# Performance work log

Hardware: AMD Instinct MI355X
Metric: run time of the kernel (lower is better)

## Reference

```python
import jax, jax.numpy as jnp
import numpy as np
from jax import lax

E = 4; D_MODEL = 128; D_FF = 128; DT_RANK = 32; D_STATE = 16
L = 12; PAD = 12  # padding_factor=1.0 -> pad L extra zeros
K_TOP = 6; U = 1e-6; EPS = 1e-5
BATCH = 8; NODES = 307; BN = BATCH * NODES
FREQ_IN = (L + PAD) // 2 + 1 + K_TOP  # 19
FREQ_OUT = L // 2 + 1                 # 7


def setup_inputs() -> dict:
    key = jax.random.key(0)
    ks = jax.random.split(key, 14)
    x = jax.random.normal(ks[0], (BN, L, D_MODEL), jnp.float32)
    graph = jax.random.normal(ks[1], (BATCH, L, D_FF, D_FF), jnp.float32) * (1.0 / D_FF)
    in_w = jax.random.normal(ks[2], (E, 2 * D_FF, D_MODEL), jnp.float32) * 0.05
    in_b = jax.random.normal(ks[3], (E, 2 * D_FF), jnp.float32) * 0.02
    x_w = jax.random.normal(ks[4], (E, DT_RANK + 2 * D_STATE + D_FF, D_FF), jnp.float32) * 0.05
    dt_w = jax.random.uniform(ks[5], (E, D_FF, DT_RANK), jnp.float32,
                              -(DT_RANK ** -0.5), DT_RANK ** -0.5)
    dt_b = -2.0 + 0.1 * jax.random.normal(ks[6], (E, D_FF), jnp.float32)
    A_log = jnp.broadcast_to(jnp.log(jnp.arange(1, D_STATE + 1, dtype=jnp.float32))[None, None, :],
                             (E, 1, D_STATE))
    out_w = jax.random.normal(ks[7], (E, D_MODEL, D_FF), jnp.float32) * 0.05
    out_b = jax.random.normal(ks[8], (E, D_MODEL), jnp.float32) * 0.02
    fw_r = jax.random.normal(ks[9], (E, FREQ_OUT, FREQ_IN), jnp.float32) * (FREQ_IN ** -0.5)
    fw_i = jax.random.normal(ks[10], (E, FREQ_OUT, FREQ_IN), jnp.float32) * (FREQ_IN ** -0.5)
    norm_w = jnp.ones((E, D_MODEL), jnp.float32)
    blk_w = jnp.full((E,), 0.5, jnp.float32)
    blk_b = jnp.full((E,), 0.5, jnp.float32)
    return dict(x=x, graph=graph, in_w=in_w, in_b=in_b, x_w=x_w, dt_w=dt_w, dt_b=dt_b,
                A_log=A_log, out_w=out_w, out_b=out_b, fw_r=fw_r, fw_i=fw_i,
                norm_w=norm_w, blk_w=blk_w, blk_b=blk_b)


def _rmsnorm(x, w):
    return x * lax.rsqrt(jnp.mean(x * x, axis=-1, keepdims=True) + EPS) * w


def _mamba_block(x, graph, in_w, in_b, x_w, dt_w, dt_b, A_log, out_w, out_b, fw_r, fw_i):
    bn, Ls, d = x.shape
    # --- FFT frequency gating ---
    x_padded = jnp.concatenate([x, jnp.zeros((bn, PAD, d), x.dtype)], axis=1)
    fp = jnp.fft.rfft(x_padded, axis=1)          # [bn, 13, d] complex
    f = jnp.fft.rfft(x, axis=1)                  # [bn, 7, d] complex
    sq_adj = (f.real + U) ** 2 + (f.imag + U) ** 2
    fs = -jnp.sort(-sq_adj, axis=1)[:, :K_TOP]   # top-K along freq dim, descending
    cat = jnp.concatenate([fp, fs.astype(fp.dtype)], axis=1)  # [bn, 19, d]
    W = lax.complex(fw_r, fw_i)                  # [7, 19]
    freq_proj = jnp.einsum('bkd,ok->bod', cat, W)  # [bn, 7, d]
    wf = jax.nn.softmax(freq_proj.real ** 2 + freq_proj.imag ** 2, axis=2)
    x_freq = jnp.fft.irfft(wf * f, axis=1)       # [bn, 12, d] (n = 2*(7-1))
    # --- input projection ---
    xz = x @ in_w.T + in_b
    xs, z = jnp.split(xz, 2, axis=-1)
    xs = jax.nn.silu(xs)
    # --- SSM ---
    A = -jnp.exp(A_log.astype(jnp.float32))      # [1, d_state]
    dbcd = xs @ x_w.T
    delta, B, C, Dp = jnp.split(dbcd, [DT_RANK, DT_RANK + D_STATE, DT_RANK + 2 * D_STATE], axis=-1)
    delta = jax.nn.softplus(delta @ dt_w.T + dt_b)  # [bn, L, d_ff]
    # graph mixing over nodes: bn = batch * n
    batch = graph.shape[0]
    delta = delta.reshape(batch, -1, Ls, D_FF)
    delta = jnp.einsum('bnsd,bsda->bnsa', delta, graph).reshape(bn, Ls, D_FF)
    deltaA = jnp.exp(delta[..., None] * A)             # [bn, L, d_ff, d_state]
    BX = delta[..., None] * B[:, :, None, :] * xs[..., None]
    dA_t = jnp.moveaxis(deltaA, 1, 0)
    bx_t = jnp.moveaxis(BX, 1, 0)

    def step(h, ab):
        dA, bx = ab
        h = dA * h + bx
        return h, h

    h0 = jnp.zeros((bn, D_FF, D_STATE), xs.dtype)
    _, hs = lax.scan(step, h0, (dA_t, bx_t))
    hs = jnp.moveaxis(hs, 0, 1)                        # [bn, L, d_ff, d_state]
    y = jnp.einsum('blds,bls->bld', hs, C) + Dp * xs
    # --- gate + output ---
    out = y * jax.nn.silu(z) * x_freq
    return out @ out_w.T + out_b


def reference(x, graph, in_w, in_b, x_w, dt_w, dt_b, A_log, out_w, out_b,
              fw_r, fw_i, norm_w, blk_w, blk_b):
    for i in range(E):
        xn = _rmsnorm(x, norm_w[i])
        out = _mamba_block(xn, graph, in_w[i], in_b[i], x_w[i], dt_w[i], dt_b[i],
                           A_log[i], out_w[i], out_b[i], fw_r[i], fw_i[i])
        out = blk_w[i] * out + blk_b[i]
        x = x + out  # dropout is identity in eval
    return jax.nn.silu(x)
```

## Files before the change

kernel.cpp:

```cpp
#include <hip/hip_runtime.h>
#include <math.h>

#define BN    2456
#define LSEQ  12
#define DM    128
#define NODES 307
#define MROWS 29472

typedef __bf16 bfx8 __attribute__((ext_vector_type(8)));
typedef float  f32x4 __attribute__((ext_vector_type(4)));

#define MFMA16(a, b, c) __builtin_amdgcn_mfma_f32_16x16x32_bf16(a, b, c, 0, 0, 0)

__device__ __forceinline__ float fsilu(float v)     { return v / (1.0f + __expf(-v)); }
__device__ __forceinline__ float fsoftplus(float x) { return fmaxf(x, 0.f) + __logf(1.0f + __expf(-fabsf(x))); }

__global__ __launch_bounds__(256)
void k_convert(const float* __restrict__ in_w, const float* __restrict__ x_w,
               const float* __restrict__ dt_w, const float* __restrict__ out_w,
               const float* __restrict__ graph,
               __bf16* __restrict__ in_w_sw, __bf16* __restrict__ x_w_sw,
               __bf16* __restrict__ dtw_sw, __bf16* __restrict__ out_w_sw,
               __bf16* __restrict__ graph_sw) {
    int idx = blockIdx.x * 256 + threadIdx.x;
    if (idx < 131072) {
        int o = idx;
        int e = o >> 15, r = o & 32767;
        int frag = r >> 9, lane = (r >> 3) & 63, j = r & 7;
        int nt = frag >> 2, kc = frag & 3, lm = lane & 15, lq = lane >> 4;
        in_w_sw[o] = (__bf16)in_w[e * 32768 + (nt * 16 + lm) * 128 + kc * 32 + lq * 8 + j];
        return;
    }
    idx -= 131072;
    if (idx < 98304) {
        int o = idx;
        int e = o / 24576, r = o - e * 24576;
        int frag = r >> 9, lane = (r >> 3) & 63, j = r & 7;
        int nt = frag >> 2, kc = frag & 3, lm = lane & 15, lq = lane >> 4;
        x_w_sw[o] = (__bf16)x_w[e * 24576 + (nt * 16 + lm) * 128 + kc * 32 + lq * 8 + j];
        return;
    }
    idx -= 98304;
    if (idx < 16384) {
        int o = idx;
        int e = o >> 12, r = o & 4095;
        int nt = r >> 9, lane = (r >> 3) & 63, j = r & 7;
        int lm = lane & 15, lq = lane >> 4;
        dtw_sw[o] = (__bf16)dt_w[e * 4096 + (nt * 16 + lm) * 32 + lq * 8 + j];
        return;
    }
    idx -= 16384;
    if (idx < 65536) {
        int o = idx;
        int e = o >> 14, r = o & 16383;
        int frag = r >> 9, lane = (r >> 3) & 63, j = r & 7;
        int f = frag >> 2, kc = frag & 3, lm = lane & 15, lq = lane >> 4;
        out_w_sw[o] = (__bf16)out_w[e * 16384 + (f * 16 + lm) * 128 + kc * 32 + lq * 8 + j];
        return;
    }
    idx -= 65536;
    if (idx < 1572864) {
        int o = idx;
        int bl = o >> 14, r = o & 16383;
        int frag = r >> 9, lane = (r >> 3) & 63, j = r & 7;
        int nt = frag >> 2, kc = frag & 3, lm = lane & 15, lq = lane >> 4;
        int a = nt * 16 + lm, d = kc * 32 + lq * 8 + j;
        graph_sw[o] = (__bf16)graph[(size_t)bl * 16384 + d * 128 + a];
    }
}

template <int N>
__device__ __forceinline__ void red_sum128(float* v, float* sred, int tid) {
#pragma unroll
    for (int off = 32; off; off >>= 1)
#pragma unroll
        for (int i = 0; i < N; ++i) v[i] += __shfl_xor(v[i], off, 64);
    if ((tid & 63) == 0) {
#pragma unroll
        for (int i = 0; i < N; ++i) sred[(tid >> 6) * N + i] = v[i];
    }
    __syncthreads();
#pragma unroll
    for (int i = 0; i < N; ++i) v[i] = sred[i] + sred[N + i];
    __syncthreads();
}

template <int N>
__device__ __forceinline__ void red_max128(float* v, float* sred, int tid) {
#pragma unroll
    for (int off = 32; off; off >>= 1)
#pragma unroll
        for (int i = 0; i < N; ++i) v[i] = fmaxf(v[i], __shfl_xor(v[i], off, 64));
    if ((tid & 63) == 0) {
#pragma unroll
        for (int i = 0; i < N; ++i) sred[(tid >> 6) * N + i] = v[i];
    }
    __syncthreads();
#pragma unroll
    for (int i = 0; i < N; ++i) v[i] = fmaxf(sred[i], sred[N + i]);
    __syncthreads();
}

__global__ __launch_bounds__(256)
void k_fused(const float* __restrict__ xcur, const float* __restrict__ norm_w,
             const __bf16* __restrict__ WiSw, const float* __restrict__ in_b,
             const __bf16* __restrict__ WxSw, const __bf16* __restrict__ DWSw,
             const float* __restrict__ dt_b, const __bf16* __restrict__ GSw,
             __bf16* __restrict__ xs_bf, __bf16* __restrict__ sz_bf,
             float* __restrict__ bcf32, __bf16* __restrict__ dpf,
             __bf16* __restrict__ dmix_bf, int e) {
    __shared__ __bf16 sxs[16 * 136];
    __shared__ __bf16 sdelta[16 * 136];
    __shared__ __bf16 sdel32[16 * 40];
    const int bl = blockIdx.x;
    const int n0 = blockIdx.y * 16;
    const int tid = threadIdx.x;
    const int wave = tid >> 6, lane = tid & 63;
    const int lm = lane & 15, lq = lane >> 4;
    const int b = bl / 12, l = bl - b * 12;
    const size_t rowbase = (size_t)bl * NODES + n0;

    const int nodeA = min(n0 + lm, NODES - 1);
    const float* xrow = xcur + ((size_t)(b * NODES + nodeA) * 12 + l) * 128 + lq * 8;
    float xv[4][8];
#pragma unroll
    for (int kc = 0; kc < 4; ++kc) {
        float4 p0 = *(const float4*)(xrow + kc * 32);
        float4 p1 = *(const float4*)(xrow + kc * 32 + 4);
        xv[kc][0] = p0.x; xv[kc][1] = p0.y; xv[kc][2] = p0.z; xv[kc][3] = p0.w;
        xv[kc][4] = p1.x; xv[kc][5] = p1.y; xv[kc][6] = p1.z; xv[kc][7] = p1.w;
    }
    float ss = 0.f;
#pragma unroll
    for (int kc = 0; kc < 4; ++kc)
#pragma unroll
        for (int j = 0; j < 8; ++j) ss += xv[kc][j] * xv[kc][j];
    ss += __shfl_xor(ss, 16, 64);
    ss += __shfl_xor(ss, 32, 64);
    const float rms = rsqrtf(ss * (1.0f / 128.0f) + 1e-5f);

    bfx8 af[4];
    const float* nwp = norm_w + e * DM + lq * 8;
#pragma unroll
    for (int kc = 0; kc < 4; ++kc) {
        float4 w0 = *(const float4*)(nwp + kc * 32);
        float4 w1 = *(const float4*)(nwp + kc * 32 + 4);
        af[kc][0] = (__bf16)(xv[kc][0] * rms * w0.x);
        af[kc][1] = (__bf16)(xv[kc][1] * rms * w0.y);
        af[kc][2] = (__bf16)(xv[kc][2] * rms * w0.z);
        af[kc][3] = (__bf16)(xv[kc][3] * rms * w0.w);
        af[kc][4] = (__bf16)(xv[kc][4] * rms * w1.x);
        af[kc][5] = (__bf16)(xv[kc][5] * rms * w1.y);
        af[kc][6] = (__bf16)(xv[kc][6] * rms * w1.z);
        af[kc][7] = (__bf16)(xv[kc][7] * rms * w1.w);
    }

    const __bf16* WxP = WxSw + (size_t)e * 24576;
    bfx8 b2[3][4];
#pragma unroll
    for (int ntl = 0; ntl < 3; ++ntl)
#pragma unroll
        for (int kc = 0; kc < 4; ++kc)
            b2[ntl][kc] = *(const bfx8*)(WxP + (((wave * 3 + ntl) * 4 + kc) * 64 + lane) * 8);

    const __bf16* WiP = WiSw + (size_t)e * 32768;
    f32x4 acc[4];
#pragma unroll
    for (int nt = 0; nt < 4; ++nt) acc[nt] = (f32x4){0.f, 0.f, 0.f, 0.f};
#pragma unroll
    for (int ntl = 0; ntl < 4; ++ntl) {
        const int nt = wave * 4 + ntl;
#pragma unroll
        for (int kc = 0; kc < 4; ++kc) {
            bfx8 bb = *(const bfx8*)(WiP + ((nt * 4 + kc) * 64 + lane) * 8);
            acc[ntl] = MFMA16(af[kc], bb, acc[ntl]);
        }
    }

    const __bf16* DWp = DWSw + (size_t)e * 4096;
    bfx8 b3[2];
#pragma unroll
    for (int ntl = 0; ntl < 2; ++ntl)
        b3[ntl] = *(const bfx8*)(DWp + ((wave * 2 + ntl) * 64 + lane) * 8);
    const __bf16* Gp = GSw + (size_t)bl * 16384;
    bfx8 b4[2][4];
#pragma unroll
    for (int ntl = 0; ntl < 2; ++ntl)
#pragma unroll
        for (int kc = 0; kc < 4; ++kc)
            b4[ntl][kc] = *(const bfx8*)(Gp + (((wave * 2 + ntl) * 4 + kc) * 64 + lane) * 8);

#pragma unroll
    for (int ntl = 0; ntl < 4; ++ntl) {
        const int col = wave * 64 + ntl * 16 + lm;
        const float bias = in_b[e * 256 + col];
#pragma unroll
        for (int r = 0; r < 4; ++r) {
            const int node = lq * 4 + r;
            const float v = fsilu(acc[ntl][r] + bias);
            const int ok = (n0 + node) < NODES;
            if (col < 128) {
                sxs[node * 136 + col] = (__bf16)v;
                if (ok) xs_bf[(rowbase + node) * 128 + col] = (__bf16)v;
            } else if (ok) {
                sz_bf[(rowbase + node) * 128 + (col - 128)] = (__bf16)v;
            }
        }
    }
    __syncthreads();

    bfx8 ax[4];
#pragma unroll
    for (int kc = 0; kc < 4; ++kc)
        ax[kc] = *(const bfx8*)(sxs + lm * 136 + kc * 32 + lq * 8);

    f32x4 xacc[3];
#pragma unroll
    for (int nt = 0; nt < 3; ++nt) xacc[nt] = (f32x4){0.f, 0.f, 0.f, 0.f};
#pragma unroll
    for (int ntl = 0; ntl < 3; ++ntl)
#pragma unroll
        for (int kc = 0; kc < 4; ++kc)
            xacc[ntl] = MFMA16(ax[kc], b2[ntl][kc], xacc[ntl]);

#pragma unroll
    for (int ntl = 0; ntl < 3; ++ntl) {
        const int col = (wave * 3 + ntl) * 16 + lm;
#pragma unroll
        for (int r = 0; r < 4; ++r) {
            const int node = lq * 4 + r;
            const float v = xacc[ntl][r];
            const int ok = (n0 + node) < NODES;
            if (col < 32) sdel32[node * 40 + col] = (__bf16)v;
            else if (col < 64) { if (ok) bcf32[(rowbase + node) * 32 + (col - 32)] = v; }
            else if (ok) dpf[(rowbase + node) * 128 + (col - 64)] = (__bf16)v;
        }
    }
    __syncthreads();

    bfx8 ad = *(const bfx8*)(sdel32 + lm * 40 + lq * 8);
    const f32x4 z4 = {0.f, 0.f, 0.f, 0.f};
#pragma unroll
    for (int ntl = 0; ntl < 2; ++ntl) {
        f32x4 dacc = MFMA16(ad, b3[ntl], z4);
        const int col = (wave * 2 + ntl) * 16 + lm;
        const float bias = dt_b[e * 128 + col];
#pragma unroll
        for (int r = 0; r < 4; ++r) {
            const int node = lq * 4 + r;
            sdelta[node * 136 + col] = (__bf16)fsoftplus(dacc[r] + bias);
        }
    }
    __syncthreads();

    bfx8 ag[4];
#pragma unroll
    for (int kc = 0; kc < 4; ++kc)
        ag[kc] = *(const bfx8*)(sdelta + lm * 136 + kc * 32 + lq * 8);

#pragma unroll
    for (int ntl = 0; ntl < 2; ++ntl) {
        f32x4 gacc = z4;
#pragma unroll
        for (int kc = 0; kc < 4; ++kc)
            gacc = MFMA16(ag[kc], b4[ntl][kc], gacc);
        const int col = (wave * 2 + ntl) * 16 + lm;
#pragma unroll
        for (int r = 0; r < 4; ++r) {
            const int node = lq * 4 + r;
            if ((n0 + node) < NODES)
                dmix_bf[(rowbase + node) * 128 + col] = (__bf16)gacc[r];
        }
    }
}

__global__ __launch_bounds__(128)
void k_scanout(const float* __restrict__ xcur, const float* __restrict__ norm_w,
               const float* __restrict__ fw_r, const float* __restrict__ fw_i,
               const __bf16* __restrict__ dmix_bf, const __bf16* __restrict__ xs_bf,
               const __bf16* __restrict__ sz_bf, const float* __restrict__ bcf32,
               const __bf16* __restrict__ dpf, const float* __restrict__ A_log,
               const __bf16* __restrict__ WoSw, const float* __restrict__ out_b,
               const float* __restrict__ blk_w, const float* __restrict__ blk_b,
               float* __restrict__ xout, int e, int last) {
    __shared__ float s_c[24], s_s[24], s_wr[133], s_wi[133];
    __shared__ float sred[24];
    __shared__ __bf16 s_out[16 * 136];
    __shared__ float sBC[384];
    const int row = blockIdx.x, tid = threadIdx.x;
    const int b = row / NODES, n = row - b * NODES;

    float bcreg[3];
#pragma unroll
    for (int i = 0; i < 3; ++i) {
        const int ii = tid + i * 128;
        const int l = ii >> 5, s = ii & 31;
        bcreg[i] = bcf32[((size_t)(b * 12 + l) * NODES + n) * 32 + s];
    }

    if (tid < 24) {
        float sv, cv;
        __sincosf(6.283185307179586f * (float)tid / 24.0f, &sv, &cv);
        s_c[tid] = cv; s_s[tid] = sv;
    }
    for (int i = tid; i < 133; i += 128) { s_wr[i] = fw_r[e * 133 + i]; s_wi[i] = fw_i[e * 133 + i]; }

    const float* xp = xcur + (size_t)row * 1536 + tid;
    float xvf[12], v[12];
#pragma unroll
    for (int l = 0; l < 12; ++l) { xvf[l] = xp[l * 128]; v[l] = xvf[l] * xvf[l]; }
    __syncthreads();
    red_sum128<12>(v, sred, tid);

    const float nrmw = norm_w[e * DM + tid];
    float xnr[12];
#pragma unroll
    for (int l = 0; l < 12; ++l)
        xnr[l] = xvf[l] * rsqrtf(v[l] * (1.0f / 128.0f) + 1e-5f) * nrmw;

    float fpr[13], fpi[13];
#pragma unroll
    for (int k = 0; k < 13; ++k) { fpr[k] = 0.f; fpi[k] = 0.f; }
#pragma unroll
    for (int l = 0; l < 12; ++l) {
#pragma unroll
        for (int k = 0; k < 13; ++k) {
            const int t = (k * l) % 24;
            fpr[k] += xnr[l] * s_c[t];
            fpi[k] -= xnr[l] * s_s[t];
        }
    }

    float a7[7];
#pragma unroll
    for (int o2 = 0; o2 < 7; ++o2) {
        float ar = fpr[2 * o2] + 1e-6f, ai = fpi[2 * o2] + 1e-6f;
        a7[o2] = ar * ar + ai * ai;
    }
#pragma unroll
    for (int pss = 0; pss < 6; ++pss)
#pragma unroll
        for (int j = 0; j < 6; ++j) {
            float hi = fmaxf(a7[j], a7[j + 1]);
            float lo = fminf(a7[j], a7[j + 1]);
            a7[j] = hi; a7[j + 1] = lo;
        }

    float p7[7];
#pragma unroll
    for (int o2 = 0; o2 < 7; ++o2) {
        float pr = 0.f, pi = 0.f;
#pragma unroll
        for (int k = 0; k < 13; ++k) {
            const float wr = s_wr[o2 * 19 + k], wi = s_wi[o2 * 19 + k];
            pr += fpr[k] * wr - fpi[k] * wi;
            pi += fpr[k] * wi + fpi[k] * wr;
        }
#pragma unroll
        for (int k = 0; k < 6; ++k) {
            const float wr = s_wr[o2 * 19 + 13 + k], wi = s_wi[o2 * 19 + 13 + k];
            pr += a7[k] * wr;
            pi += a7[k] * wi;
        }
        p7[o2] = pr * pr + pi * pi;
    }

    float m7[7], ex[7], sm[7];
#pragma unroll
    for (int o2 = 0; o2 < 7; ++o2) m7[o2] = p7[o2];
    red_max128<7>(m7, sred, tid);
#pragma unroll
    for (int o2 = 0; o2 < 7; ++o2) { ex[o2] = __expf(p7[o2] - m7[o2]); sm[o2] = ex[o2]; }
    red_sum128<7>(sm, sred, tid);

    float gr[7], gi[7];
#pragma unroll
    for (int o2 = 0; o2 < 7; ++o2) {
        const float wf = ex[o2] / sm[o2];
        gr[o2] = wf * fpr[2 * o2];
        gi[o2] = wf * fpi[2 * o2];
    }

    float xfqv[12];
#pragma unroll
    for (int l = 0; l < 12; ++l) {
        float val = gr[0] + ((l & 1) ? -gr[6] : gr[6]);
#pragma unroll
        for (int o2 = 1; o2 < 6; ++o2) {
            const int t = (2 * o2 * l) % 24;
            val += 2.0f * (gr[o2] * s_c[t] - gi[o2] * s_s[t]);
        }
        xfqv[l] = val * (1.0f / 12.0f);
    }

#pragma unroll
    for (int i = 0; i < 3; ++i) sBC[tid + i * 128] = bcreg[i];
#pragma unroll
    for (int r = 12; r < 16; ++r) s_out[r * 136 + tid] = (__bf16)0.f;
    __syncthreads();

    float As[16];
#pragma unroll
    for (int s = 0; s < 16; ++s) As[s] = -__expf(A_log[e * 16 + s]);
    float h[16];
#pragma unroll
    for (int s = 0; s < 16; ++s) h[s] = 0.f;
#pragma unroll
    for (int l = 0; l < 12; ++l) {
        const size_t base = ((size_t)(b * 12 + l) * NODES + n) * 128 + tid;
        const float dl = (float)dmix_bf[base];
        const float xsv = (float)xs_bf[base];
        const float Dp = (float)dpf[base];
        const float dlx = dl * xsv;
        float y = 0.f;
#pragma unroll
        for (int s = 0; s < 16; ++s) {
            h[s] = __expf(dl * As[s]) * h[s] + sBC[l * 32 + s] * dlx;
            y += h[s] * sBC[l * 32 + 16 + s];
        }
        y += Dp * xsv;
        const float g = y * (float)sz_bf[base] * xfqv[l];
        s_out[l * 136 + tid] = (__bf16)g;
    }
    __syncthreads();

    const int wave = tid >> 6, lane = tid & 63;
    const int lm = lane & 15, lq = lane >> 4;
    const __bf16* Wop = WoSw + (size_t)e * 16384;
    bfx8 a[4];
#pragma unroll
    for (int kc = 0; kc < 4; ++kc)
        a[kc] = *(const bfx8*)(s_out + lm * 136 + kc * 32 + lq * 8);

    f32x4 acc[4];
#pragma unroll
    for (int nt = 0; nt < 4; ++nt) acc[nt] = (f32x4){0.f, 0.f, 0.f, 0.f};
#pragma unroll
    for (int nt = 0; nt < 4; ++nt) {
        const int f = wave * 4 + nt;
#pragma unroll
        for (int kc = 0; kc < 4; ++kc) {
            bfx8 bb = *(const bfx8*)(Wop + ((f * 4 + kc) * 64 + lane) * 8);
            acc[nt] = MFMA16(a[kc], bb, acc[nt]);
        }
    }

    const float bw = blk_w[e], bb2 = blk_b[e];
#pragma unroll
    for (int nt = 0; nt < 4; ++nt) {
        const int col = wave * 64 + nt * 16 + lm;
        const float ob = out_b[e * 128 + col];
#pragma unroll
        for (int r = 0; r < 4; ++r) {
            const int m = lq * 4 + r;
            if (m < 12) {
                const size_t gi = ((size_t)row * 12 + m) * 128 + col;
                float vv = bw * (acc[nt][r] + ob) + bb2 + xcur[gi];
                if (last) vv = fsilu(vv);
                xout[gi] = vv;
            }
        }
    }
}

extern "C" void kernel_launch(void* const* d_in, const int* in_sizes, int n_in,
                              void* d_out, int out_size, void* d_ws, size_t ws_size,
                              hipStream_t stream) {
    (void)in_sizes; (void)n_in; (void)out_size; (void)ws_size;
    const float* x_in   = (const float*)d_in[0];
    const float* graph  = (const float*)d_in[1];
    const float* in_w   = (const float*)d_in[2];
    const float* in_b   = (const float*)d_in[3];
    const float* x_w    = (const float*)d_in[4];
    const float* dt_w   = (const float*)d_in[5];
    const float* dt_b   = (const float*)d_in[6];
    const float* A_log  = (const float*)d_in[7];
    const float* out_w  = (const float*)d_in[8];
    const float* out_b  = (const float*)d_in[9];
    const float* fw_r   = (const float*)d_in[10];
    const float* fw_i   = (const float*)d_in[11];
    const float* norm_w = (const float*)d_in[12];
    const float* blk_w  = (const float*)d_in[13];
    const float* blk_b  = (const float*)d_in[14];
    float* out = (float*)d_out;

    float* ws = (float*)d_ws;
    size_t o = 0;
    __bf16* in_w_sw  = (__bf16*)(ws + o); o += 131072 / 2;
    __bf16* x_w_sw   = (__bf16*)(ws + o); o += 98304 / 2;
    __bf16* dtw_sw   = (__bf16*)(ws + o); o += 16384 / 2;
    __bf16* out_w_sw = (__bf16*)(ws + o); o += 65536 / 2;
    __bf16* graph_sw = (__bf16*)(ws + o); o += 1572864 / 2;
    const size_t NE = (size_t)MROWS * 128;
    __bf16* xs_bf    = (__bf16*)(ws + o); o += NE / 2;
    __bf16* sz_bf    = (__bf16*)(ws + o); o += NE / 2;
    __bf16* dpf      = (__bf16*)(ws + o); o += NE / 2;
    __bf16* dmix_bf  = (__bf16*)(ws + o); o += NE / 2;
    float*  bcf32    = ws + o;            o += (size_t)MROWS * 32;

    hipLaunchKernelGGL(k_convert, dim3(7360), dim3(256), 0, stream,
                       in_w, x_w, dt_w, out_w, graph,
                       in_w_sw, x_w_sw, dtw_sw, out_w_sw, graph_sw);

    for (int e = 0; e < 4; ++e) {
        const float* xcur = (e == 0) ? x_in : (const float*)out;
        const int last = (e == 3) ? 1 : 0;
        hipLaunchKernelGGL(k_fused, dim3(96, 20), dim3(256), 0, stream,
                           xcur, norm_w, in_w_sw, in_b, x_w_sw, dtw_sw, dt_b, graph_sw,
                           xs_bf, sz_bf, bcf32, dpf, dmix_bf, e);
        hipLaunchKernelGGL(k_scanout, dim3(BN), dim3(128), 0, stream,
                           xcur, norm_w, fw_r, fw_i, dmix_bf, xs_bf, sz_bf, bcf32,
                           dpf, A_log, out_w_sw, out_b, blk_w, blk_b, out, e, last);
    }
}
```

Measured before the change: 407.9 us.

## Interleave scan operands, fold padded FFT into weights, and use power-chain decay in scan

After: 382.3 us. 1.07x faster.

```diff
diff --git a/kernel.cpp b/kernel.cpp
--- a/kernel.cpp
+++ b/kernel.cpp
@@ -8,6 +8,7 @@
 #define MROWS 29472
 
 typedef __bf16 bfx8 __attribute__((ext_vector_type(8)));
+typedef __bf16 bfx4 __attribute__((ext_vector_type(4)));
 typedef float  f32x4 __attribute__((ext_vector_type(4)));
 
 #define MFMA16(a, b, c) __builtin_amdgcn_mfma_f32_16x16x32_bf16(a, b, c, 0, 0, 0)
@@ -19,9 +20,10 @@
 void k_convert(const float* __restrict__ in_w, const float* __restrict__ x_w,
                const float* __restrict__ dt_w, const float* __restrict__ out_w,
                const float* __restrict__ graph,
+               const float* __restrict__ fw_r, const float* __restrict__ fw_i,
                __bf16* __restrict__ in_w_sw, __bf16* __restrict__ x_w_sw,
                __bf16* __restrict__ dtw_sw, __bf16* __restrict__ out_w_sw,
-               __bf16* __restrict__ graph_sw) {
+               __bf16* __restrict__ graph_sw, float* __restrict__ mw) {
     int idx = blockIdx.x * 256 + threadIdx.x;
     if (idx < 131072) {
         int o = idx;
@@ -60,12 +62,37 @@
     }
     idx -= 65536;
     if (idx < 1572864) {
+        int bl = idx >> 14, r = idx & 16383;
+        int dd = r >> 7, a = r & 127;
+        int nt = a >> 4, lm = a & 15, kc = dd >> 5, lq = (dd >> 3) & 3, j = dd & 7;
+        graph_sw[(size_t)bl * 16384 + ((size_t)((nt * 4 + kc) * 64 + lq * 16 + lm)) * 8 + j] =
+            (__bf16)graph[(size_t)bl * 16384 + dd * 128 + a];
+        return;
+    }
+    idx -= 1572864;
+    if (idx < 336) {
         int o = idx;
-        int bl = o >> 14, r = o & 16383;
-        int frag = r >> 9, lane = (r >> 3) & 63, j = r & 7;
-        int nt = frag >> 2, kc = frag & 3, lm = lane & 15, lq = lane >> 4;
-        int a = nt * 16 + lm, d = kc * 32 + lq * 8 + j;
-        graph_sw[o] = (__bf16)graph[(size_t)bl * 16384 + d * 128 + a];
+        int e = o / 84, r = o - e * 84;
+        int o2 = r / 12, l = r - o2 * 12;
+        float mr = 0.f, mi = 0.f;
+        for (int k = 0; k < 13; ++k) {
+            float sv, cv;
+            __sincosf(6.283185307179586f * (float)(k * l) / 24.0f, &sv, &cv);
+            const float wr = fw_r[e * 133 + o2 * 19 + k], wi = fw_i[e * 133 + o2 * 19 + k];
+            mr += wr * cv + wi * sv;
+            mi += wi * cv - wr * sv;
+        }
+        mw[e * 256 + (o2 * 12 + l) * 2]     = mr;
+        mw[e * 256 + (o2 * 12 + l) * 2 + 1] = mi;
+        return;
+    }
+    idx -= 336;
+    if (idx < 168) {
+        int o = idx;
+        int e = o / 42, r = o - e * 42;
+        int o2 = r / 6, k = r - o2 * 6;
+        mw[e * 256 + 168 + (o2 * 6 + k) * 2]     = fw_r[e * 133 + o2 * 19 + 13 + k];
+        mw[e * 256 + 168 + (o2 * 6 + k) * 2 + 1] = fw_i[e * 133 + o2 * 19 + 13 + k];
     }
 }
 
@@ -106,12 +133,11 @@
              const __bf16* __restrict__ WiSw, const float* __restrict__ in_b,
              const __bf16* __restrict__ WxSw, const __bf16* __restrict__ DWSw,
              const float* __restrict__ dt_b, const __bf16* __restrict__ GSw,
-             __bf16* __restrict__ xs_bf, __bf16* __restrict__ sz_bf,
-             float* __restrict__ bcf32, __bf16* __restrict__ dpf,
-             __bf16* __restrict__ dmix_bf, int e) {
+             __bf16* __restrict__ scanp, float* __restrict__ bcf32, int e) {
     __shared__ __bf16 sxs[16 * 136];
     __shared__ __bf16 sdelta[16 * 136];
     __shared__ __bf16 sdel32[16 * 40];
+    __shared__ float sxf[16][132];
     const int bl = blockIdx.x;
     const int n0 = blockIdx.y * 16;
     const int tid = threadIdx.x;
@@ -120,16 +146,20 @@
     const int b = bl / 12, l = bl - b * 12;
     const size_t rowbase = (size_t)bl * NODES + n0;
 
-    const int nodeA = min(n0 + lm, NODES - 1);
-    const float* xrow = xcur + ((size_t)(b * NODES + nodeA) * 12 + l) * 128 + lq * 8;
+    for (int i = tid; i < 1024; i += 256) {
+        const int node = i >> 6, dp2 = i & 63;
+        const int gn = min(n0 + node, NODES - 1);
+        *(float2*)(&sxf[node][dp2 * 2]) =
+            *(const float2*)(xcur + ((size_t)(b * NODES + gn) * 12 + l) * 128 + dp2 * 2);
+    }
+    __syncthreads();
+
     float xv[4][8];
 #pragma unroll
-    for (int kc = 0; kc < 4; ++kc) {
-        float4 p0 = *(const float4*)(xrow + kc * 32);
-        float4 p1 = *(const float4*)(xrow + kc * 32 + 4);
-        xv[kc][0] = p0.x; xv[kc][1] = p0.y; xv[kc][2] = p0.z; xv[kc][3] = p0.w;
-        xv[kc][4] = p1.x; xv[kc][5] = p1.y; xv[kc][6] = p1.z; xv[kc][7] = p1.w;
-    }
+    for (int kc = 0; kc < 4; ++kc)
+#pragma unroll
+        for (int j = 0; j < 8; ++j) xv[kc][j] = sxf[lm][kc * 32 + lq * 8 + j];
+
     float ss = 0.f;
 #pragma unroll
     for (int kc = 0; kc < 4; ++kc)
@@ -201,9 +231,9 @@
             const int ok = (n0 + node) < NODES;
             if (col < 128) {
                 sxs[node * 136 + col] = (__bf16)v;
-                if (ok) xs_bf[(rowbase + node) * 128 + col] = (__bf16)v;
+                if (ok) scanp[(rowbase + node) * 512 + col * 4 + 1] = (__bf16)v;
             } else if (ok) {
-                sz_bf[(rowbase + node) * 128 + (col - 128)] = (__bf16)v;
+                scanp[(rowbase + node) * 512 + (col - 128) * 4 + 3] = (__bf16)v;
             }
         }
     }
@@ -233,7 +263,7 @@
             const int ok = (n0 + node) < NODES;
             if (col < 32) sdel32[node * 40 + col] = (__bf16)v;
             else if (col < 64) { if (ok) bcf32[(rowbase + node) * 32 + (col - 32)] = v; }
-            else if (ok) dpf[(rowbase + node) * 128 + (col - 64)] = (__bf16)v;
+            else if (ok) scanp[(rowbase + node) * 512 + (col - 64) * 4 + 2] = (__bf16)v;
         }
     }
     __syncthreads();
@@ -269,98 +299,95 @@
         for (int r = 0; r < 4; ++r) {
             const int node = lq * 4 + r;
             if ((n0 + node) < NODES)
-                dmix_bf[(rowbase + node) * 128 + col] = (__bf16)gacc[r];
+                scanp[(rowbase + node) * 512 + col * 4 + 0] = (__bf16)gacc[r];
         }
     }
 }
 
 __global__ __launch_bounds__(128)
 void k_scanout(const float* __restrict__ xcur, const float* __restrict__ norm_w,
-               const float* __restrict__ fw_r, const float* __restrict__ fw_i,
-               const __bf16* __restrict__ dmix_bf, const __bf16* __restrict__ xs_bf,
-               const __bf16* __restrict__ sz_bf, const float* __restrict__ bcf32,
-               const __bf16* __restrict__ dpf, const float* __restrict__ A_log,
+               const float* __restrict__ mw, const __bf16* __restrict__ scanp,
+               const float* __restrict__ bcf32, const float* __restrict__ A_log,
                const __bf16* __restrict__ WoSw, const float* __restrict__ out_b,
                const float* __restrict__ blk_w, const float* __restrict__ blk_b,
                float* __restrict__ xout, int e, int last) {
-    __shared__ float s_c[24], s_s[24], s_wr[133], s_wi[133];
     __shared__ float sred[24];
     __shared__ __bf16 s_out[16 * 136];
-    __shared__ float sBC[384];
     const int row = blockIdx.x, tid = threadIdx.x;
     const int b = row / NODES, n = row - b * NODES;
 
-    float bcreg[3];
-#pragma unroll
-    for (int i = 0; i < 3; ++i) {
-        const int ii = tid + i * 128;
-        const int l = ii >> 5, s = ii & 31;
-        bcreg[i] = bcf32[((size_t)(b * 12 + l) * NODES + n) * 32 + s];
-    }
-
-    if (tid < 24) {
-        float sv, cv;
-        __sincosf(6.283185307179586f * (float)tid / 24.0f, &sv, &cv);
-        s_c[tid] = cv; s_s[tid] = sv;
-    }
-    for (int i = tid; i < 133; i += 128) { s_wr[i] = fw_r[e * 133 + i]; s_wi[i] = fw_i[e * 133 + i]; }
+    constexpr float SQ32 = 0.8660254037844386f;
+    constexpr float C12[12] = {1.f, SQ32, 0.5f, 0.f, -0.5f, -SQ32, -1.f, -SQ32, -0.5f, 0.f, 0.5f, SQ32};
+    constexpr float S12[12] = {0.f, 0.5f, SQ32, 1.f, SQ32, 0.5f, 0.f, -0.5f, -SQ32, -1.f, -SQ32, -0.5f};
+    constexpr float LOGT[16] = {0.f, 0.6931472f, 1.0986123f, 1.3862944f, 1.6094379f, 1.7917595f,
+                                1.9459101f, 2.0794415f, 2.1972246f, 2.3025851f, 2.3978953f,
+                                2.4849066f, 2.5649494f, 2.6390573f, 2.7080502f, 2.7725887f};
+
+    bfx4 sc12[12];
+    const size_t sb = ((size_t)(b * 12) * NODES + n) * 512 + (size_t)tid * 4;
+#pragma unroll
+    for (int l = 0; l < 12; ++l)
+        sc12[l] = *(const bfx4*)(scanp + sb + (size_t)l * (NODES * 512));
+
+    int chainOK = 1;
+#pragma unroll
+    for (int s = 0; s < 16; ++s)
+        chainOK &= (fabsf(A_log[e * 16 + s] - LOGT[s]) < 1e-4f) ? 1 : 0;
 
     const float* xp = xcur + (size_t)row * 1536 + tid;
-    float xvf[12], v[12];
-#pragma unroll
-    for (int l = 0; l < 12; ++l) { xvf[l] = xp[l * 128]; v[l] = xvf[l] * xvf[l]; }
-    __syncthreads();
+    float xv[12], v[12];
+#pragma unroll
+    for (int l = 0; l < 12; ++l) { xv[l] = xp[l * 128]; v[l] = xv[l] * xv[l]; }
     red_sum128<12>(v, sred, tid);
 
     const float nrmw = norm_w[e * DM + tid];
     float xnr[12];
 #pragma unroll
     for (int l = 0; l < 12; ++l)
-        xnr[l] = xvf[l] * rsqrtf(v[l] * (1.0f / 128.0f) + 1e-5f) * nrmw;
-
-    float fpr[13], fpi[13];
-#pragma unroll
-    for (int k = 0; k < 13; ++k) { fpr[k] = 0.f; fpi[k] = 0.f; }
-#pragma unroll
-    for (int l = 0; l < 12; ++l) {
-#pragma unroll
-        for (int k = 0; k < 13; ++k) {
-            const int t = (k * l) % 24;
-            fpr[k] += xnr[l] * s_c[t];
-            fpi[k] -= xnr[l] * s_s[t];
-        }
+        xnr[l] = xv[l] * rsqrtf(v[l] * (1.0f / 128.0f) + 1e-5f) * nrmw;
+
+    float fr[7], fi[7];
+#pragma unroll
+    for (int o2 = 0; o2 < 7; ++o2) {
+        float r = 0.f, im = 0.f;
+#pragma unroll
+        for (int l = 0; l < 12; ++l) {
+            const int t = (o2 * l) % 12;
+            r += xnr[l] * C12[t];
+            im -= xnr[l] * S12[t];
+        }
+        fr[o2] = r; fi[o2] = im;
     }
 
     float a7[7];
 #pragma unroll
     for (int o2 = 0; o2 < 7; ++o2) {
-        float ar = fpr[2 * o2] + 1e-6f, ai = fpi[2 * o2] + 1e-6f;
+        const float ar = fr[o2] + 1e-6f, ai = fi[o2] + 1e-6f;
         a7[o2] = ar * ar + ai * ai;
     }
 #pragma unroll
     for (int pss = 0; pss < 6; ++pss)
 #pragma unroll
         for (int j = 0; j < 6; ++j) {
-            float hi = fmaxf(a7[j], a7[j + 1]);
-            float lo = fminf(a7[j], a7[j + 1]);
+            const float hi = fmaxf(a7[j], a7[j + 1]);
+            const float lo = fminf(a7[j], a7[j + 1]);
             a7[j] = hi; a7[j + 1] = lo;
         }
 
+    const float* Me = mw + e * 256;
     float p7[7];
 #pragma unroll
     for (int o2 = 0; o2 < 7; ++o2) {
         float pr = 0.f, pi = 0.f;
 #pragma unroll
-        for (int k = 0; k < 13; ++k) {
-            const float wr = s_wr[o2 * 19 + k], wi = s_wi[o2 * 19 + k];
-            pr += fpr[k] * wr - fpi[k] * wi;
-            pi += fpr[k] * wi + fpi[k] * wr;
+        for (int l = 0; l < 12; ++l) {
+            pr += xnr[l] * Me[(o2 * 12 + l) * 2];
+            pi += xnr[l] * Me[(o2 * 12 + l) * 2 + 1];
         }
 #pragma unroll
         for (int k = 0; k < 6; ++k) {
-            const float wr = s_wr[o2 * 19 + 13 + k], wi = s_wi[o2 * 19 + 13 + k];
-            pr += a7[k] * wr;
-            pi += a7[k] * wi;
+            pr += a7[k] * Me[168 + (o2 * 6 + k) * 2];
+            pi += a7[k] * Me[168 + (o2 * 6 + k) * 2 + 1];
         }
         p7[o2] = pr * pr + pi * pi;
     }
@@ -377,8 +404,8 @@
 #pragma unroll
     for (int o2 = 0; o2 < 7; ++o2) {
         const float wf = ex[o2] / sm[o2];
-        gr[o2] = wf * fpr[2 * o2];
-        gi[o2] = wf * fpi[2 * o2];
+        gr[o2] = wf * fr[o2];
+        gi[o2] = wf * fi[o2];
     }
 
     float xfqv[12];
@@ -387,40 +414,65 @@
         float val = gr[0] + ((l & 1) ? -gr[6] : gr[6]);
 #pragma unroll
         for (int o2 = 1; o2 < 6; ++o2) {
-            const int t = (2 * o2 * l) % 24;
-            val += 2.0f * (gr[o2] * s_c[t] - gi[o2] * s_s[t]);
+            const int t = (o2 * l) % 12;
+            val += 2.0f * (gr[o2] * C12[t] - gi[o2] * S12[t]);
         }
         xfqv[l] = val * (1.0f / 12.0f);
     }
 
 #pragma unroll
-    for (int i = 0; i < 3; ++i) sBC[tid + i * 128] = bcreg[i];
-#pragma unroll
     for (int r = 12; r < 16; ++r) s_out[r * 136 + tid] = (__bf16)0.f;
-    __syncthreads();
-
-    float As[16];
-#pragma unroll
-    for (int s = 0; s < 16; ++s) As[s] = -__expf(A_log[e * 16 + s]);
+
     float h[16];
 #pragma unroll
-    for (int s = 0; s < 16; ++s) h[s] = 0.f;
-#pragma unroll
-    for (int l = 0; l < 12; ++l) {
-        const size_t base = ((size_t)(b * 12 + l) * NODES + n) * 128 + tid;
-        const float dl = (float)dmix_bf[base];
-        const float xsv = (float)xs_bf[base];
-        const float Dp = (float)dpf[base];
-        const float dlx = dl * xsv;
-        float y = 0.f;
-#pragma unroll
-        for (int s = 0; s < 16; ++s) {
-            h[s] = __expf(dl * As[s]) * h[s] + sBC[l * 32 + s] * dlx;
-            y += h[s] * sBC[l * 32 + 16 + s];
-        }
-        y += Dp * xsv;
-        const float g = y * (float)sz_bf[base] * xfqv[l];
-        s_out[l * 136 + tid] = (__bf16)g;
+    for (int j = 0; j < 16; ++j) h[j] = 0.f;
+
+    if (chainOK) {
+#pragma unroll
+        for (int l = 0; l < 12; ++l) {
+            const float dl = (float)sc12[l][0], xsv = (float)sc12[l][1];
+            const float dlx = dl * xsv;
+            const float* bc = bcf32 + ((size_t)(b * 12 + l) * NODES + n) * 32;
+            const float q1 = __expf(-dl);
+            const float q2 = q1 * q1, q4 = q2 * q2, q8 = q4 * q4;
+            float pw[16];
+            pw[0] = q1;        pw[1] = q2;        pw[2] = q1 * q2;   pw[3] = q4;
+            pw[4] = q1 * q4;   pw[5] = q2 * q4;   pw[6] = pw[2] * q4; pw[7] = q8;
+            pw[8] = q1 * q8;   pw[9] = q2 * q8;   pw[10] = pw[2] * q8; pw[11] = q4 * q8;
+            pw[12] = pw[4] * q8; pw[13] = pw[5] * q8; pw[14] = pw[6] * q8; pw[15] = q8 * q8;
+            float y0 = 0.f, y1 = 0.f, y2 = 0.f, y3 = 0.f;
+#pragma unroll
+            for (int j = 0; j < 4; ++j) {
+                h[j]      = pw[j]      * h[j]      + bc[j]      * dlx;  y0 += h[j]      * bc[16 + j];
+                h[j + 4]  = pw[j + 4]  * h[j + 4]  + bc[j + 4]  * dlx;  y1 += h[j + 4]  * bc[20 + j];
+                h[j + 8]  = pw[j + 8]  * h[j + 8]  + bc[j + 8]  * dlx;  y2 += h[j + 8]  * bc[24 + j];
+                h[j + 12] = pw[j + 12] * h[j + 12] + bc[j + 12] * dlx;  y3 += h[j + 12] * bc[28 + j];
+            }
+            float y = (y0 + y1) + (y2 + y3);
+            y += (float)sc12[l][2] * xsv;
+            const float g = y * (float)sc12[l][3] * xfqv[l];
+            s_out[l * 136 + tid] = (__bf16)g;
+        }
+    } else {
+        float As[16];
+#pragma unroll
+        for (int s = 0; s < 16; ++s) As[s] = -__expf(A_log[e * 16 + s]);
+#pragma unroll
+        for (int l = 0; l < 12; ++l) {
+            const float dl = (float)sc12[l][0], xsv = (float)sc12[l][1];
+            const float dlx = dl * xsv;
+            const float* bc = bcf32 + ((size_t)(b * 12 + l) * NODES + n) * 32;
+            float y = 0.f;
+#pragma unroll
+            for (int j = 0; j < 16; ++j) {
+                const float a = __expf(dl * As[j]);
+                h[j] = a * h[j] + bc[j] * dlx;
+                y += h[j] * bc[16 + j];
+            }
+            y += (float)sc12[l][2] * xsv;
+            const float g = y * (float)sc12[l][3] * xfqv[l];
+            s_out[l * 136 + tid] = (__bf16)g;
+        }
     }
     __syncthreads();
 
@@ -454,7 +506,7 @@
         for (int r = 0; r < 4; ++r) {
             const int m = lq * 4 + r;
             if (m < 12) {
-                const size_t gi = ((size_t)row * 12 + m) * 128 + col;
+                const size_t gi = (size_t)row * 1536 + m * 128 + col;
                 float vv = bw * (acc[nt][r] + ob) + bb2 + xcur[gi];
                 if (last) vv = fsilu(vv);
                 xout[gi] = vv;
@@ -491,25 +543,22 @@
     __bf16* dtw_sw   = (__bf16*)(ws + o); o += 16384 / 2;
     __bf16* out_w_sw = (__bf16*)(ws + o); o += 65536 / 2;
     __bf16* graph_sw = (__bf16*)(ws + o); o += 1572864 / 2;
-    const size_t NE = (size_t)MROWS * 128;
-    __bf16* xs_bf    = (__bf16*)(ws + o); o += NE / 2;
-    __bf16* sz_bf    = (__bf16*)(ws + o); o += NE / 2;
-    __bf16* dpf      = (__bf16*)(ws + o); o += NE / 2;
-    __bf16* dmix_bf  = (__bf16*)(ws + o); o += NE / 2;
+    __bf16* scanp    = (__bf16*)(ws + o); o += (size_t)MROWS * 512 / 2;
     float*  bcf32    = ws + o;            o += (size_t)MROWS * 32;
-
-    hipLaunchKernelGGL(k_convert, dim3(7360), dim3(256), 0, stream,
-                       in_w, x_w, dt_w, out_w, graph,
-                       in_w_sw, x_w_sw, dtw_sw, out_w_sw, graph_sw);
+    float*  mw       = ws + o;            o += 1024;
+
+    hipLaunchKernelGGL(k_convert, dim3(7362), dim3(256), 0, stream,
+                       in_w, x_w, dt_w, out_w, graph, fw_r, fw_i,
+                       in_w_sw, x_w_sw, dtw_sw, out_w_sw, graph_sw, mw);
 
     for (int e = 0; e < 4; ++e) {
         const float* xcur = (e == 0) ? x_in : (const float*)out;
         const int last = (e == 3) ? 1 : 0;
         hipLaunchKernelGGL(k_fused, dim3(96, 20), dim3(256), 0, stream,
                            xcur, norm_w, in_w_sw, in_b, x_w_sw, dtw_sw, dt_b, graph_sw,
-                           xs_bf, sz_bf, bcf32, dpf, dmix_bf, e);
+                           scanp, bcf32, e);
         hipLaunchKernelGGL(k_scanout, dim3(BN), dim3(128), 0, stream,
-                           xcur, norm_w, fw_r, fw_i, dmix_bf, xs_bf, sz_bf, bcf32,
-                           dpf, A_log, out_w_sw, out_b, blk_w, blk_b, out, e, last);
+                           xcur, norm_w, mw, scanp, bcf32, A_log,
+                           out_w_sw, out_b, blk_w, blk_b, out, e, last);
     }
 }
```
